# Kernel optimization log

Hardware: AMD Instinct MI355X
Metric: run time of the kernel (lower is better)

The kernel has to match this reference:

```python
import jax, jax.numpy as jnp
import numpy as np

K = 3  # kernel_size
P = 1  # padding (must satisfy K == 2*P+1 for the original einsum to be shape-valid)


def setup_inputs() -> dict:
    key = jax.random.key(0)
    k1, k2, k3 = jax.random.split(key, 3)
    b, i, c, L, o = 16, 64, 4, 4096, 64
    x = jax.random.normal(k1, (b, i, c, L), dtype=jnp.float32)
    time_tensor = jax.random.uniform(k2, (b, c, L), dtype=jnp.float32)
    weights = jax.random.normal(k3, (o, i, c, K), dtype=jnp.float32)
    return {"x": x, "time_tensor": time_tensor, "weights": weights}


def reference(x, time_tensor, weights):
    """x: (b,i,c,L), time_tensor: (b,c,L), weights: (o,i,c,K) -> (b,o,c,L).

    Faithful to the torch module: pad x/time by P on the time axis, unfold x
    into sliding windows, pad the unfolded tensor again by P, multiply by the
    time scalar per (b,c,l) and contract over (i,k), then crop P from each end.
    The time factor is scalar per output element, so we factor it out of the
    einsum instead of materializing the (b,o,i,c,k,l) dynamic_weights tensor --
    mathematically identical, massively cheaper.
    """
    xp = jnp.pad(x, ((0, 0), (0, 0), (0, 0), (P, P)))            # (b,i,c,L+2P)
    tp = jnp.pad(time_tensor, ((0, 0), (0, 0), (P, P)))          # (b,c,L+2P)
    Lw = xp.shape[-1] - K + 1                                    # == L since K=2P+1
    # unfold -> (b,i,c,K,Lw), matching torch's permute(0,2,1,4,3) after transpose
    xu = jnp.stack([xp[..., j:j + Lw] for j in range(K)], axis=-2)
    xu = jnp.transpose(xu, (0, 2, 1, 3, 4))                      # (b,c,i,K,Lw)
    xu = jnp.pad(xu, ((0, 0), (0, 0), (0, 0), (0, 0), (P, P)))   # (b,c,i,K,Lw+2P)
    conv = jnp.einsum('oick,bcikl->bocl', weights, xu)           # (b,o,c,L+2P)
    out = conv * tp[:, None, :, :]
    return out[..., P:-P]                                        # (b,o,c,L)
```

## Files before the change

kernel.cpp:

```cpp
#include <hip/hip_runtime.h>


#define NB 16
#define NI 64
#define NC 4
#define NL 4096
#define NO 64
#define KW 3
#define LT 64
#define NT 2
#define ROWS (LT + 2)
#define ROWB 128

#define W_PACK_BYTES (NO * NI * NC * KW * 2)

typedef float f32x4 __attribute__((ext_vector_type(4)));
typedef short bf16x8 __attribute__((ext_vector_type(8)));
typedef unsigned int u32x2 __attribute__((ext_vector_type(2)));

__device__ inline unsigned short f2bf(float f) {
    unsigned int u = __builtin_bit_cast(unsigned int, f);
    u += 0x7FFFu + ((u >> 16) & 1u);
    return (unsigned short)(u >> 16);
}

__global__ __launch_bounds__(256)
void prepack_w_kernel(const float* __restrict__ w, unsigned short* __restrict__ wp) {
    const int idx = blockIdx.x * 256 + threadIdx.x;
    const float v = w[idx];
    const int k = idx % 3;
    int r = idx / 3;
    const int c = r & 3;  r >>= 2;
    const int i = r & 63;
    const int o = r >> 6;
    const int cc   = k * 2 + (i >> 5);
    const int lane = (((i >> 3) & 3) << 4) | (o & 15);
    const int j    = i & 7;
    const int wv   = o >> 4;
    wp[(((c * 4 + wv) * 6 + cc) * 64 + lane) * 8 + j] = f2bf(v);
}

__device__ __forceinline__ void load_x(const float* __restrict__ xb, int lb,
                                       int t, int lane, int wave,
                                       float s[16], float& h) {
    const int l = lb + lane;
#pragma unroll
    for (int it = 0; it < 4; ++it) {
        const int ib = (it * 4 + wave) * 4;
        const float* xi = xb + (size_t)ib * (NC * NL);
        s[it * 4 + 0] = xi[l];
        s[it * 4 + 1] = xi[(size_t)(NC * NL) + l];
        s[it * 4 + 2] = xi[(size_t)(2 * NC * NL) + l];
        s[it * 4 + 3] = xi[(size_t)(3 * NC * NL) + l];
    }
    h = 0.f;
    if (t < 128) {
        const int which = t & 1;
        const int i     = t >> 1;
        const int lh    = which ? (lb + LT) : (lb - 1);
        if (lh >= 0 && lh < NL) h = xb[(size_t)i * (NC * NL) + lh];
    }
}

__device__ __forceinline__ void write_lds(char* __restrict__ buf,
                                          int t, int lane, int wave,
                                          const float s[16], float h) {
    const int rr  = lane + 1;
    const int swz = (rr & 7) << 4;
#pragma unroll
    for (int it = 0; it < 4; ++it) {
        const int ib = (it * 4 + wave) * 4;
        u32x2 pk;
        pk[0] = (unsigned int)f2bf(s[it * 4 + 0]) | ((unsigned int)f2bf(s[it * 4 + 1]) << 16);
        pk[1] = (unsigned int)f2bf(s[it * 4 + 2]) | ((unsigned int)f2bf(s[it * 4 + 3]) << 16);
        *(u32x2*)(buf + rr * ROWB + ((2 * ib) ^ swz)) = pk;
    }
    if (t < 128) {
        const int which = t & 1;
        const int i     = t >> 1;
        const int row   = which ? (LT + 1) : 0;
        *(unsigned short*)(buf + row * ROWB + ((2 * i) ^ ((row & 7) << 4))) = f2bf(h);
    }
}

__device__ __forceinline__ void compute_store(const char* __restrict__ buf,
                                              const bf16x8 wfrag[6],
                                              const float* __restrict__ tb,
                                              float* __restrict__ ob,
                                              int lb, int lane) {
    const int lcol  = lane & 15;
    const int ksub2 = (lane >> 4) * 16;

    f32x4 tv[4];
#pragma unroll
    for (int lt = 0; lt < 4; ++lt)
        tv[lt] = *(const f32x4*)(tb + lb + lt * 16 + (lane >> 4) * 4);

    f32x4 acc[4] = {};
#pragma unroll
    for (int lt = 0; lt < 4; ++lt) {
#pragma unroll
        for (int cc = 0; cc < 6; ++cc) {
            const int k    = cc >> 1;
            const int ih   = cc & 1;
            const int row  = lt * 16 + lcol + k;
            const int colb = ih * 64 + ksub2;
            const int off  = row * ROWB + (colb ^ ((row & 7) << 4));
            const bf16x8 xf = *(const bf16x8*)(buf + off);
            acc[lt] = __builtin_amdgcn_mfma_f32_16x16x32_bf16(xf, wfrag[cc], acc[lt], 0, 0, 0);
        }
    }
#pragma unroll
    for (int lt = 0; lt < 4; ++lt) {
        const int l0 = lb + lt * 16 + (lane >> 4) * 4;
        f32x4 r;
#pragma unroll
        for (int q = 0; q < 4; ++q) r[q] = acc[lt][q] * tv[lt][q];
        *(f32x4*)(ob + l0) = r;
    }
}

__global__ __launch_bounds__(256)
void tconv_mfma_kernel(const float* __restrict__ x,
                       const float* __restrict__ tt,
                       const unsigned short* __restrict__ wp,
                       float* __restrict__ out)
{
    __shared__ char lds[NT][ROWS * ROWB];

    const int t    = threadIdx.x;
    const int lane = t & 63;
    const int wave = t >> 6;
    const int c    = blockIdx.y;
    const int b    = blockIdx.z;
    const int lb0  = blockIdx.x * (LT * NT);
    const int lb1  = lb0 + LT;
    const int o0   = wave * 16;

    bf16x8 wfrag[6];
    {
        const bf16x8* wpb = (const bf16x8*)wp + (size_t)((c * 4 + wave) * 6) * 64 + lane;
#pragma unroll
        for (int cc = 0; cc < 6; ++cc) wfrag[cc] = wpb[cc * 64];
    }

    const float* xb = x + ((size_t)b * NI * NC + c) * NL;
    const float* tb = tt + (size_t)(b * NC + c) * NL;
    float* ob = out + ((size_t)b * NO * NC + (size_t)(o0 + (lane & 15)) * NC + c) * NL;

    float s0[16], h0;
    load_x(xb, lb0, t, lane, wave, s0, h0);
    write_lds(&lds[0][0], t, lane, wave, s0, h0);
    __syncthreads();

    float s1[16], h1;
    load_x(xb, lb1, t, lane, wave, s1, h1);

    compute_store(&lds[0][0], wfrag, tb, ob, lb0, lane);

    write_lds(&lds[1][0], t, lane, wave, s1, h1);
    __syncthreads();
    compute_store(&lds[1][0], wfrag, tb, ob, lb1, lane);
}

extern "C" void kernel_launch(void* const* d_in, const int* in_sizes, int n_in,
                              void* d_out, int out_size, void* d_ws, size_t ws_size,
                              hipStream_t stream) {
    const float* x  = (const float*)d_in[0];
    const float* tt = (const float*)d_in[1];
    const float* w  = (const float*)d_in[2];
    float* out = (float*)d_out;
    unsigned short* wpck = (unsigned short*)d_ws;

    dim3 block(256);
    prepack_w_kernel<<<dim3(NO * NI * NC * KW / 256), block, 0, stream>>>(w, wpck);

    dim3 grid(NL / (LT * NT), NC, NB);
    tconv_mfma_kernel<<<grid, block, 0, stream>>>(x, tt, wpck, out);
}
```

Measured before the change: 37.32 us.

## Process four L-tiles per block with a single shared halo and vectorized x loads

```diff
diff --git a/kernel.cpp b/kernel.cpp
--- a/kernel.cpp
+++ b/kernel.cpp
@@ -8,8 +8,9 @@
 #define NO 64
 #define KW 3
 #define LT 64
-#define NT 2
-#define ROWS (LT + 2)
+#define NT 4
+#define LBLK (LT * NT)
+#define ROWS (LBLK + 2)
 #define ROWB 128
 
 #define W_PACK_BYTES (NO * NI * NC * KW * 2)
@@ -40,61 +41,40 @@
     wp[(((c * 4 + wv) * 6 + cc) * 64 + lane) * 8 + j] = f2bf(v);
 }
 
-__device__ __forceinline__ void load_x(const float* __restrict__ xb, int lb,
-                                       int t, int lane, int wave,
-                                       float s[16], float& h) {
-    const int l = lb + lane;
+__device__ __forceinline__ void stage_load(const float* __restrict__ xb,
+                                           int l0, int g, f32x4 s[4]) {
+    const float* p = xb + (size_t)(4 * g) * (NC * NL) + l0;
+    s[0] = *(const f32x4*)(p);
+    s[1] = *(const f32x4*)(p + NC * NL);
+    s[2] = *(const f32x4*)(p + 2 * NC * NL);
+    s[3] = *(const f32x4*)(p + 3 * NC * NL);
+}
+
+__device__ __forceinline__ void stage_write(char* __restrict__ lds,
+                                            int r0, int g, const f32x4 s[4]) {
 #pragma unroll
-    for (int it = 0; it < 4; ++it) {
-        const int ib = (it * 4 + wave) * 4;
-        const float* xi = xb + (size_t)ib * (NC * NL);
-        s[it * 4 + 0] = xi[l];
-        s[it * 4 + 1] = xi[(size_t)(NC * NL) + l];
-        s[it * 4 + 2] = xi[(size_t)(2 * NC * NL) + l];
-        s[it * 4 + 3] = xi[(size_t)(3 * NC * NL) + l];
-    }
-    h = 0.f;
-    if (t < 128) {
-        const int which = t & 1;
-        const int i     = t >> 1;
-        const int lh    = which ? (lb + LT) : (lb - 1);
-        if (lh >= 0 && lh < NL) h = xb[(size_t)i * (NC * NL) + lh];
+    for (int r = 0; r < 4; ++r) {
+        const int rr = r0 + r;
+        u32x2 pk;
+        pk[0] = (unsigned int)f2bf(s[0][r]) | ((unsigned int)f2bf(s[1][r]) << 16);
+        pk[1] = (unsigned int)f2bf(s[2][r]) | ((unsigned int)f2bf(s[3][r]) << 16);
+        *(u32x2*)(lds + rr * ROWB + ((8 * g) ^ ((rr & 7) << 4))) = pk;
     }
 }
 
-__device__ __forceinline__ void write_lds(char* __restrict__ buf,
-                                          int t, int lane, int wave,
-                                          const float s[16], float h) {
-    const int rr  = lane + 1;
-    const int swz = (rr & 7) << 4;
-#pragma unroll
-    for (int it = 0; it < 4; ++it) {
-        const int ib = (it * 4 + wave) * 4;
-        u32x2 pk;
-        pk[0] = (unsigned int)f2bf(s[it * 4 + 0]) | ((unsigned int)f2bf(s[it * 4 + 1]) << 16);
-        pk[1] = (unsigned int)f2bf(s[it * 4 + 2]) | ((unsigned int)f2bf(s[it * 4 + 3]) << 16);
-        *(u32x2*)(buf + rr * ROWB + ((2 * ib) ^ swz)) = pk;
-    }
-    if (t < 128) {
-        const int which = t & 1;
-        const int i     = t >> 1;
-        const int row   = which ? (LT + 1) : 0;
-        *(unsigned short*)(buf + row * ROWB + ((2 * i) ^ ((row & 7) << 4))) = f2bf(h);
-    }
-}
-
-__device__ __forceinline__ void compute_store(const char* __restrict__ buf,
+__device__ __forceinline__ void compute_store(const char* __restrict__ lds,
                                               const bf16x8 wfrag[6],
                                               const float* __restrict__ tb,
                                               float* __restrict__ ob,
-                                              int lb, int lane) {
+                                              int t, int lb0, int lane) {
     const int lcol  = lane & 15;
     const int ksub2 = (lane >> 4) * 16;
+    const int lbt   = lb0 + t * LT;
 
     f32x4 tv[4];
 #pragma unroll
     for (int lt = 0; lt < 4; ++lt)
-        tv[lt] = *(const f32x4*)(tb + lb + lt * 16 + (lane >> 4) * 4);
+        tv[lt] = *(const f32x4*)(tb + lbt + lt * 16 + (lane >> 4) * 4);
 
     f32x4 acc[4] = {};
 #pragma unroll
@@ -103,16 +83,16 @@
         for (int cc = 0; cc < 6; ++cc) {
             const int k    = cc >> 1;
             const int ih   = cc & 1;
-            const int row  = lt * 16 + lcol + k;
+            const int row  = t * LT + lt * 16 + lcol + k;
             const int colb = ih * 64 + ksub2;
             const int off  = row * ROWB + (colb ^ ((row & 7) << 4));
-            const bf16x8 xf = *(const bf16x8*)(buf + off);
+            const bf16x8 xf = *(const bf16x8*)(lds + off);
             acc[lt] = __builtin_amdgcn_mfma_f32_16x16x32_bf16(xf, wfrag[cc], acc[lt], 0, 0, 0);
         }
     }
 #pragma unroll
     for (int lt = 0; lt < 4; ++lt) {
-        const int l0 = lb + lt * 16 + (lane >> 4) * 4;
+        const int l0 = lbt + lt * 16 + (lane >> 4) * 4;
         f32x4 r;
 #pragma unroll
         for (int q = 0; q < 4; ++q) r[q] = acc[lt][q] * tv[lt][q];
@@ -120,22 +100,24 @@
     }
 }
 
-__global__ __launch_bounds__(256)
+__global__ __launch_bounds__(256, 4)
 void tconv_mfma_kernel(const float* __restrict__ x,
                        const float* __restrict__ tt,
                        const unsigned short* __restrict__ wp,
                        float* __restrict__ out)
 {
-    __shared__ char lds[NT][ROWS * ROWB];
+    __shared__ char lds[ROWS * ROWB];
 
     const int t    = threadIdx.x;
     const int lane = t & 63;
     const int wave = t >> 6;
     const int c    = blockIdx.y;
     const int b    = blockIdx.z;
-    const int lb0  = blockIdx.x * (LT * NT);
-    const int lb1  = lb0 + LT;
+    const int lb0  = blockIdx.x * LBLK;
     const int o0   = wave * 16;
+    const int quad = lane & 15;
+    const int g    = wave * 4 + (lane >> 4);
+    const int lq   = 4 * quad;
 
     bf16x8 wfrag[6];
     {
@@ -148,19 +130,36 @@
     const float* tb = tt + (size_t)(b * NC + c) * NL;
     float* ob = out + ((size_t)b * NO * NC + (size_t)(o0 + (lane & 15)) * NC + c) * NL;
 
-    float s0[16], h0;
-    load_x(xb, lb0, t, lane, wave, s0, h0);
-    write_lds(&lds[0][0], t, lane, wave, s0, h0);
+    f32x4 s0[4], s1[4];
+    stage_load(xb, lb0 + 0 * LT + lq, g, s0);
+    stage_load(xb, lb0 + 1 * LT + lq, g, s1);
+    float h = 0.f; int hrow = 0, hcol = 0;
+    if (t < 128) {
+        const int which = t & 1;
+        const int i     = t >> 1;
+        hrow = which ? (LBLK + 1) : 0;
+        hcol = 2 * i;
+        const int lh = which ? (lb0 + LBLK) : (lb0 - 1);
+        if (lh >= 0 && lh < NL) h = xb[(size_t)i * (NC * NL) + lh];
+    }
+    stage_write(lds, 1 + 0 * LT + lq, g, s0);
+    stage_write(lds, 1 + 1 * LT + lq, g, s1);
+    if (t < 128)
+        *(unsigned short*)(lds + hrow * ROWB + (hcol ^ ((hrow & 7) << 4))) = f2bf(h);
     __syncthreads();
 
-    float s1[16], h1;
-    load_x(xb, lb1, t, lane, wave, s1, h1);
+    stage_load(xb, lb0 + 2 * LT + lq, g, s0);
+    compute_store(lds, wfrag, tb, ob, 0, lb0, lane);
+    stage_write(lds, 1 + 2 * LT + lq, g, s0);
+    __syncthreads();
 
-    compute_store(&lds[0][0], wfrag, tb, ob, lb0, lane);
+    stage_load(xb, lb0 + 3 * LT + lq, g, s1);
+    compute_store(lds, wfrag, tb, ob, 1, lb0, lane);
+    stage_write(lds, 1 + 3 * LT + lq, g, s1);
+    __syncthreads();
 
-    write_lds(&lds[1][0], t, lane, wave, s1, h1);
-    __syncthreads();
-    compute_store(&lds[1][0], wfrag, tb, ob, lb1, lane);
+    compute_store(lds, wfrag, tb, ob, 2, lb0, lane);
+    compute_store(lds, wfrag, tb, ob, 3, lb0, lane);
 }
 
 extern "C" void kernel_launch(void* const* d_in, const int* in_sizes, int n_in,
@@ -175,6 +174,6 @@
     dim3 block(256);
     prepack_w_kernel<<<dim3(NO * NI * NC * KW / 256), block, 0, stream>>>(w, wpck);
 
-    dim3 grid(NL / (LT * NT), NC, NB);
+    dim3 grid(NL / LBLK, NC, NB);
     tconv_mfma_kernel<<<grid, block, 0, stream>>>(x, tt, wpck, out);
 }
```

New measurement: 33.60 us. 10.0% less time.

## Give each wave all output channels and a private double-buffered L strip

Applied to the files above, without the earlier changes.

```diff
diff --git a/kernel.cpp b/kernel.cpp
--- a/kernel.cpp
+++ b/kernel.cpp
@@ -7,16 +7,20 @@
 #define NL 4096
 #define NO 64
 #define KW 3
-#define LT 64
-#define NT 2
-#define ROWS (LT + 2)
+#define CL 32
+#define NCH 4
+#define WL (CL * NCH)
+#define WAVES 2
+#define BLKL (WL * WAVES)
+#define BROWS (CL + 2)
 #define ROWB 128
+#define BUFB (BROWS * ROWB)
 
 #define W_PACK_BYTES (NO * NI * NC * KW * 2)
 
 typedef float f32x4 __attribute__((ext_vector_type(4)));
 typedef short bf16x8 __attribute__((ext_vector_type(8)));
-typedef unsigned int u32x2 __attribute__((ext_vector_type(2)));
+typedef unsigned int u32x4 __attribute__((ext_vector_type(4)));
 
 __device__ inline unsigned short f2bf(float f) {
     unsigned int u = __builtin_bit_cast(unsigned int, f);
@@ -40,127 +44,132 @@
     wp[(((c * 4 + wv) * 6 + cc) * 64 + lane) * 8 + j] = f2bf(v);
 }
 
-__device__ __forceinline__ void load_x(const float* __restrict__ xb, int lb,
-                                       int t, int lane, int wave,
-                                       float s[16], float& h) {
-    const int l = lb + lane;
+__device__ __forceinline__ void stage_load(const float* __restrict__ xb,
+                                           int l0, int lane,
+                                           f32x4 v[8], float h[2]) {
+    const int q  = lane & 7;
+    const int gi = lane >> 3;
+    const float* p = xb + (size_t)(8 * gi) * (NC * NL) + l0 + 4 * q;
 #pragma unroll
-    for (int it = 0; it < 4; ++it) {
-        const int ib = (it * 4 + wave) * 4;
-        const float* xi = xb + (size_t)ib * (NC * NL);
-        s[it * 4 + 0] = xi[l];
-        s[it * 4 + 1] = xi[(size_t)(NC * NL) + l];
-        s[it * 4 + 2] = xi[(size_t)(2 * NC * NL) + l];
-        s[it * 4 + 3] = xi[(size_t)(3 * NC * NL) + l];
-    }
-    h = 0.f;
-    if (t < 128) {
-        const int which = t & 1;
-        const int i     = t >> 1;
-        const int lh    = which ? (lb + LT) : (lb - 1);
-        if (lh >= 0 && lh < NL) h = xb[(size_t)i * (NC * NL) + lh];
-    }
+    for (int ii = 0; ii < 8; ++ii)
+        v[ii] = *(const f32x4*)(p + (size_t)ii * (NC * NL));
+    const float* ph = xb + (size_t)lane * (NC * NL);
+    h[0] = (l0 - 1 >= 0) ? ph[l0 - 1] : 0.f;
+    h[1] = (l0 + CL < NL) ? ph[l0 + CL] : 0.f;
 }
 
-__device__ __forceinline__ void write_lds(char* __restrict__ buf,
-                                          int t, int lane, int wave,
-                                          const float s[16], float h) {
-    const int rr  = lane + 1;
-    const int swz = (rr & 7) << 4;
+__device__ __forceinline__ void stage_write(char* __restrict__ buf, int lane,
+                                            const f32x4 v[8], const float h[2]) {
+    const int q  = lane & 7;
+    const int gi = lane >> 3;
 #pragma unroll
-    for (int it = 0; it < 4; ++it) {
-        const int ib = (it * 4 + wave) * 4;
-        u32x2 pk;
-        pk[0] = (unsigned int)f2bf(s[it * 4 + 0]) | ((unsigned int)f2bf(s[it * 4 + 1]) << 16);
-        pk[1] = (unsigned int)f2bf(s[it * 4 + 2]) | ((unsigned int)f2bf(s[it * 4 + 3]) << 16);
-        *(u32x2*)(buf + rr * ROWB + ((2 * ib) ^ swz)) = pk;
+    for (int r = 0; r < 4; ++r) {
+        const int row = 4 * q + r + 1;
+        u32x4 pk;
+#pragma unroll
+        for (int w2 = 0; w2 < 4; ++w2)
+            pk[w2] = (unsigned int)f2bf(v[2 * w2][r]) |
+                     ((unsigned int)f2bf(v[2 * w2 + 1][r]) << 16);
+        *(u32x4*)(buf + row * ROWB + ((16 * gi) ^ ((row & 7) << 4))) = pk;
     }
-    if (t < 128) {
-        const int which = t & 1;
-        const int i     = t >> 1;
-        const int row   = which ? (LT + 1) : 0;
-        *(unsigned short*)(buf + row * ROWB + ((2 * i) ^ ((row & 7) << 4))) = f2bf(h);
-    }
+    *(unsigned short*)(buf + 0 * ROWB + (2 * lane)) = f2bf(h[0]);
+    *(unsigned short*)(buf + 33 * ROWB + ((2 * lane) ^ 16)) = f2bf(h[1]);
 }
 
-__device__ __forceinline__ void compute_store(const char* __restrict__ buf,
-                                              const bf16x8 wfrag[6],
+__device__ __forceinline__ void compute_chunk(const char* __restrict__ buf,
+                                              const bf16x8 wfrag[4][6],
                                               const float* __restrict__ tb,
-                                              float* __restrict__ ob,
-                                              int lb, int lane) {
+                                              float* __restrict__ outb,
+                                              int l0, int lane) {
     const int lcol  = lane & 15;
     const int ksub2 = (lane >> 4) * 16;
 
-    f32x4 tv[4];
+    f32x4 tv[2];
 #pragma unroll
-    for (int lt = 0; lt < 4; ++lt)
-        tv[lt] = *(const f32x4*)(tb + lb + lt * 16 + (lane >> 4) * 4);
+    for (int lt = 0; lt < 2; ++lt)
+        tv[lt] = *(const f32x4*)(tb + l0 + lt * 16 + (lane >> 4) * 4);
 
-    f32x4 acc[4] = {};
+    f32x4 acc[2][4] = {};
 #pragma unroll
-    for (int lt = 0; lt < 4; ++lt) {
+    for (int lt = 0; lt < 2; ++lt) {
 #pragma unroll
         for (int cc = 0; cc < 6; ++cc) {
             const int k    = cc >> 1;
             const int ih   = cc & 1;
             const int row  = lt * 16 + lcol + k;
-            const int colb = ih * 64 + ksub2;
-            const int off  = row * ROWB + (colb ^ ((row & 7) << 4));
+            const int off  = row * ROWB + ((ih * 64 + ksub2) ^ ((row & 7) << 4));
             const bf16x8 xf = *(const bf16x8*)(buf + off);
-            acc[lt] = __builtin_amdgcn_mfma_f32_16x16x32_bf16(xf, wfrag[cc], acc[lt], 0, 0, 0);
+#pragma unroll
+            for (int s = 0; s < 4; ++s)
+                acc[lt][s] = __builtin_amdgcn_mfma_f32_16x16x32_bf16(
+                    xf, wfrag[s][cc], acc[lt][s], 0, 0, 0);
         }
     }
 #pragma unroll
-    for (int lt = 0; lt < 4; ++lt) {
-        const int l0 = lb + lt * 16 + (lane >> 4) * 4;
-        f32x4 r;
+    for (int s = 0; s < 4; ++s) {
+        float* os = outb + (size_t)(s * 16 + lcol) * (NC * NL);
 #pragma unroll
-        for (int q = 0; q < 4; ++q) r[q] = acc[lt][q] * tv[lt][q];
-        *(f32x4*)(ob + l0) = r;
+        for (int lt = 0; lt < 2; ++lt) {
+            const int lq = l0 + lt * 16 + (lane >> 4) * 4;
+            f32x4 r;
+#pragma unroll
+            for (int q = 0; q < 4; ++q) r[q] = acc[lt][s][q] * tv[lt][q];
+            *(f32x4*)(os + lq) = r;
+        }
     }
 }
 
-__global__ __launch_bounds__(256)
+__global__ __launch_bounds__(128, 2)
 void tconv_mfma_kernel(const float* __restrict__ x,
                        const float* __restrict__ tt,
                        const unsigned short* __restrict__ wp,
                        float* __restrict__ out)
 {
-    __shared__ char lds[NT][ROWS * ROWB];
+    __shared__ char lds[WAVES * 2 * BUFB];
 
     const int t    = threadIdx.x;
     const int lane = t & 63;
     const int wave = t >> 6;
     const int c    = blockIdx.y;
     const int b    = blockIdx.z;
-    const int lb0  = blockIdx.x * (LT * NT);
-    const int lb1  = lb0 + LT;
-    const int o0   = wave * 16;
+    const int lw0  = blockIdx.x * BLKL + wave * WL;
 
-    bf16x8 wfrag[6];
-    {
-        const bf16x8* wpb = (const bf16x8*)wp + (size_t)((c * 4 + wave) * 6) * 64 + lane;
-#pragma unroll
-        for (int cc = 0; cc < 6; ++cc) wfrag[cc] = wpb[cc * 64];
-    }
+    char* buf0 = lds + wave * 2 * BUFB;
+    char* buf1 = buf0 + BUFB;
 
     const float* xb = x + ((size_t)b * NI * NC + c) * NL;
     const float* tb = tt + (size_t)(b * NC + c) * NL;
-    float* ob = out + ((size_t)b * NO * NC + (size_t)(o0 + (lane & 15)) * NC + c) * NL;
+    float* outb = out + ((size_t)b * NO * NC + c) * NL;
 
-    float s0[16], h0;
-    load_x(xb, lb0, t, lane, wave, s0, h0);
-    write_lds(&lds[0][0], t, lane, wave, s0, h0);
-    __syncthreads();
+    f32x4 va[8]; float ha[2];
+    stage_load(xb, lw0 + 0 * CL, lane, va, ha);
 
-    float s1[16], h1;
-    load_x(xb, lb1, t, lane, wave, s1, h1);
+    bf16x8 wfrag[4][6];
+    {
+        const bf16x8* wpb = (const bf16x8*)wp + (size_t)(c * 4 * 6) * 64 + lane;
+#pragma unroll
+        for (int s = 0; s < 4; ++s)
+#pragma unroll
+            for (int cc = 0; cc < 6; ++cc)
+                wfrag[s][cc] = wpb[(s * 6 + cc) * 64];
+    }
 
-    compute_store(&lds[0][0], wfrag, tb, ob, lb0, lane);
+    stage_write(buf0, lane, va, ha);
 
-    write_lds(&lds[1][0], t, lane, wave, s1, h1);
-    __syncthreads();
-    compute_store(&lds[1][0], wfrag, tb, ob, lb1, lane);
+    f32x4 vb[8]; float hb[2];
+    stage_load(xb, lw0 + 1 * CL, lane, vb, hb);
+    compute_chunk(buf0, wfrag, tb, outb, lw0 + 0 * CL, lane);
+    stage_write(buf1, lane, vb, hb);
+
+    stage_load(xb, lw0 + 2 * CL, lane, va, ha);
+    compute_chunk(buf1, wfrag, tb, outb, lw0 + 1 * CL, lane);
+    stage_write(buf0, lane, va, ha);
+
+    stage_load(xb, lw0 + 3 * CL, lane, vb, hb);
+    compute_chunk(buf0, wfrag, tb, outb, lw0 + 2 * CL, lane);
+    stage_write(buf1, lane, vb, hb);
+
+    compute_chunk(buf1, wfrag, tb, outb, lw0 + 3 * CL, lane);
 }
 
 extern "C" void kernel_launch(void* const* d_in, const int* in_sizes, int n_in,
@@ -172,9 +181,8 @@
     float* out = (float*)d_out;
     unsigned short* wpck = (unsigned short*)d_ws;
 
-    dim3 block(256);
-    prepack_w_kernel<<<dim3(NO * NI * NC * KW / 256), block, 0, stream>>>(w, wpck);
+    prepack_w_kernel<<<dim3(NO * NI * NC * KW / 256), dim3(256), 0, stream>>>(w, wpck);
 
-    dim3 grid(NL / (LT * NT), NC, NB);
-    tconv_mfma_kernel<<<grid, block, 0, stream>>>(x, tt, wpck, out);
+    dim3 grid(NL / BLKL, NC, NB);
+    tconv_mfma_kernel<<<grid, dim3(128), 0, stream>>>(x, tt, wpck, out);
 }
```

Result: slower. 46.44 us (+24.4%).
